# Optimization experiments

Hardware: AMD Instinct MI355X
Metric: run time of the kernel (lower is better)

## Reference

```python
import jax, jax.numpy as jnp
import numpy as np

EMBED_DIM = 1024
NUM_HEADS = 16
HEAD_DIM = EMBED_DIM // NUM_HEADS


def setup_inputs() -> dict:
    key = jax.random.key(0)
    ks = jax.random.split(key, 7)
    B, S, E = 2, 2048, EMBED_DIM
    # xavier_uniform bound for square [E, E] weight
    bound = float(np.sqrt(6.0 / (E + E)))
    mkw = lambda k: jax.random.uniform(k, (E, E), jnp.float32, -bound, bound)
    return {
        "query": jax.random.normal(ks[0], (B, S, E), jnp.float32),
        "key": jax.random.normal(ks[1], (B, S, E), jnp.float32),
        "value": jax.random.normal(ks[2], (B, S, E), jnp.float32),
        "Wq": mkw(ks[3]),
        "Wk": mkw(ks[4]),
        "Wv": mkw(ks[5]),
        "Wo": mkw(ks[6]),
    }


def reference(query, key, value, Wq, Wk, Wv, Wo):
    # Chunked sigmoid attention: since sigmoid has no cross-key normalization
    # and all projections are bias-free linear maps, summing per-KV-chunk
    # partial outputs is mathematically identical to the full computation:
    #   out = (sigmoid(scale * Q K^T) @ V) @ Wo^T
    B, L, E = query.shape
    H, D = NUM_HEADS, HEAD_DIM
    scale = D ** -0.5
    q = (query @ Wq.T).reshape(B, L, H, D) * scale   # [B,L,H,D]
    k = (key @ Wk.T).reshape(B, -1, H, D)            # [B,S,H,D]
    v = (value @ Wv.T).reshape(B, -1, H, D)          # [B,S,H,D]
    scores = jax.nn.sigmoid(jnp.einsum('blhd,bshd->bhls', q, k))  # [B,H,L,S]
    o = jnp.einsum('bhls,bshd->blhd', scores, v).reshape(B, L, E)
    return o @ Wo.T
```

## Files before the change

kernel.cpp:

```cpp
#include <hip/hip_runtime.h>

typedef float f32x4 __attribute__((ext_vector_type(4)));
typedef float f32x16 __attribute__((ext_vector_type(16)));
typedef __bf16 bf16x4 __attribute__((ext_vector_type(4)));
typedef __bf16 bf16x8 __attribute__((ext_vector_type(8)));

constexpr int E = 1024;
constexpr int S = 2048;
constexpr int Bsz = 2;
constexpr int H = 16;
constexpr int Dh = 64;
constexpr int M = Bsz * S;

#define GLOAD_LDS16(g, l)                                                                 \
  __builtin_amdgcn_global_load_lds((const __attribute__((address_space(1))) void*)(g),    \
                                   (__attribute__((address_space(3))) void*)(l), 16, 0, 0)

__device__ __forceinline__ unsigned pk2(float a, float b) {
  union { __bf16 h[2]; unsigned u; } r;
  r.h[0] = (__bf16)a; r.h[1] = (__bf16)b;
  return r.u;
}

__global__ __launch_bounds__(256) void convert_bf16(
    const float* __restrict__ q, const float* __restrict__ k,
    const float* __restrict__ v, const float* __restrict__ wq,
    const float* __restrict__ wk, const float* __restrict__ wv,
    const float* __restrict__ wo, __bf16* __restrict__ aq,
    __bf16* __restrict__ ak, __bf16* __restrict__ av,
    __bf16* __restrict__ wqkv, __bf16* __restrict__ wob) {
  const int id = blockIdx.y;
  const float* src;
  __bf16* dst;
  int n;
  float scale = 1.0f;
  switch (id) {
    case 0: src = q;  dst = aq;             n = M * E; break;
    case 1: src = k;  dst = ak;             n = M * E; break;
    case 2: src = v;  dst = av;             n = M * E; break;
    case 3: src = wq; dst = wqkv;           n = E * E; scale = -0.18033688f; break;
    case 4: src = wk; dst = wqkv + E * E;   n = E * E; break;
    case 5: src = wv; dst = wqkv + 2 * E * E; n = E * E; break;
    default: src = wo; dst = wob;           n = E * E; break;
  }
  const int stride = gridDim.x * 256 * 8;
  for (int i = (blockIdx.x * 256 + threadIdx.x) * 8; i < n; i += stride) {
    f32x4 a = *reinterpret_cast<const f32x4*>(&src[i]);
    f32x4 b = *reinterpret_cast<const f32x4*>(&src[i + 4]);
    bf16x8 o;
    o[0] = (__bf16)(a[0] * scale); o[1] = (__bf16)(a[1] * scale);
    o[2] = (__bf16)(a[2] * scale); o[3] = (__bf16)(a[3] * scale);
    o[4] = (__bf16)(b[0] * scale); o[5] = (__bf16)(b[1] * scale);
    o[6] = (__bf16)(b[2] * scale); o[7] = (__bf16)(b[3] * scale);
    *reinterpret_cast<bf16x8*>(&dst[i]) = o;
  }
}

template <int TM, int MODE>
__global__ __launch_bounds__(256) void gemm_bf16nt(
    const __bf16* __restrict__ A0, const __bf16* __restrict__ A1,
    const __bf16* __restrict__ A2, const __bf16* __restrict__ Bw,
    void* __restrict__ C0, void* __restrict__ C1, void* __restrict__ C2) {
  constexpr int MI = TM / 32;
  __shared__ __bf16 As[TM][64];
  __shared__ __bf16 Bs[128][64];

  const int t    = threadIdx.x;
  const int lane = t & 63;
  const int wid  = t >> 6;
  const int wr   = (wid >> 1) * (TM / 2);
  const int wc   = (wid & 1) * 64;
  const int r16  = lane & 15;
  const int tm   = blockIdx.y * TM;
  const int tn   = blockIdx.x * 128;
  const int which = tn >> 10;

  const __bf16* Ab = (MODE == 0) ? (which == 0 ? A0 : which == 1 ? A1 : A2) : A0;

  f32x4 acc[MI][4] = {};

  for (int kt = 0; kt < E / 64; ++kt) {
    const int k0 = kt * 64;
    __syncthreads();
    constexpr int ACH = TM / 8;
    constexpr int NCH = ACH + 16;
#pragma unroll
    for (int c = wid; c < NCH; c += 4) {
      const bool isA = c < ACH;
      const int cc   = isA ? c : c - ACH;
      const int L    = cc * 1024 + lane * 16;
      const int row  = L >> 7;
      const int sw   = ((L >> 4) & 7) ^ (row & 7);
      const __bf16* src = isA ? &Ab[(size_t)(tm + row) * E + k0 + sw * 8]
                              : &Bw[(size_t)(tn + row) * E + k0 + sw * 8];
      char* dst = (isA ? (char*)As : (char*)Bs) + cc * 1024;
      GLOAD_LDS16(src, dst);
    }
    __syncthreads();
#pragma unroll
    for (int kc = 0; kc < 2; ++kc) {
      bf16x8 af[MI], bfv[4];
#pragma unroll
      for (int mi = 0; mi < MI; ++mi) {
        int row = wr + mi * 16 + r16;
        int g   = (kc * 4 + (lane >> 4)) ^ (row & 7);
        af[mi] = *reinterpret_cast<const bf16x8*>(&As[row][g * 8]);
      }
#pragma unroll
      for (int ni = 0; ni < 4; ++ni) {
        int row = wc + ni * 16 + r16;
        int g   = (kc * 4 + (lane >> 4)) ^ (row & 7);
        bfv[ni] = *reinterpret_cast<const bf16x8*>(&Bs[row][g * 8]);
      }
#pragma unroll
      for (int mi = 0; mi < MI; ++mi)
#pragma unroll
        for (int ni = 0; ni < 4; ++ni)
          acc[mi][ni] = __builtin_amdgcn_mfma_f32_16x16x32_bf16(af[mi], bfv[ni],
                                                                acc[mi][ni], 0, 0, 0);
    }
  }

#pragma unroll
  for (int mi = 0; mi < MI; ++mi) {
#pragma unroll
    for (int ni = 0; ni < 4; ++ni) {
#pragma unroll
      for (int j = 0; j < 4; ++j) {
        float v = acc[mi][ni][j];
        int m = tm + wr + mi * 16 + ((lane >> 4) << 2) + j;
        int n = tn + wc + ni * 16 + r16;
        if constexpr (MODE == 0) {
          int nl = n & 1023;
          int b = m >> 11, s = m & 2047, h = nl >> 6, d = nl & 63;
          __bf16* Cout = which == 0 ? (__bf16*)C0 : which == 1 ? (__bf16*)C1
                                                              : (__bf16*)C2;
          if (which < 2) {
            Cout[((size_t)(b * H + h) * S + s) * Dh + d] = (__bf16)v;
          } else {
            int ssw = (s & ~12) | ((s & 4) << 1) | ((s & 8) >> 1);
            Cout[((size_t)(b * H + h) * Dh + d) * S + ssw] = (__bf16)v;
          }
        } else {
          ((float*)C0)[(size_t)m * E + n] = v;
        }
      }
    }
  }
}

__global__ __launch_bounds__(256) void attn_sigmoid(const __bf16* __restrict__ Q,
                                                    const __bf16* __restrict__ K,
                                                    const __bf16* __restrict__ Vt,
                                                    __bf16* __restrict__ O) {
  __shared__ char smem[32768];

  const int t     = threadIdx.x;
  const int lane  = t & 63;
  const int wid   = t >> 6;
  const int l31   = lane & 31;
  const int hh    = lane >> 5;
  const int qgrp  = wid & 1;
  const int shalf = wid >> 1;
  const int q0    = blockIdx.x * 64;
  const int h     = blockIdx.y;
  const int b     = blockIdx.z;

  const __bf16* Qh = Q + (size_t)(b * H + h) * S * Dh;
  const __bf16* Kh = K + (size_t)(b * H + h) * S * Dh;
  const __bf16* Vh = Vt + (size_t)(b * H + h) * Dh * S;

  char* const myBase = smem + shalf * 16384;

  const __bf16* kSrc = Kh + (size_t)(shalf * 1024 + (lane >> 3)) * Dh +
                       (((lane & 7) ^ (lane >> 3)) * 8);
  const __bf16* vSrc = Vh + (size_t)(lane >> 2) * S + shalf * 1024 +
                       (((lane & 3) ^ ((lane >> 3) & 3)) * 8);

  auto stage = [&](int it, int buf) {
    char* dst = myBase + buf * 8192;
    if (qgrp == 0) {
#pragma unroll
      for (int j = 0; j < 4; ++j)
        GLOAD_LDS16(kSrc + it * 2048 + j * 512, dst + j * 1024);
    } else {
#pragma unroll
      for (int j = 0; j < 4; ++j)
        GLOAD_LDS16(vSrc + it * 32 + (size_t)j * 16 * S, dst + 4096 + j * 1024);
    }
  };

  bf16x8 Qf[4];
#pragma unroll
  for (int kc = 0; kc < 4; ++kc)
    Qf[kc] = *reinterpret_cast<const bf16x8*>(
        &Qh[(size_t)(q0 + qgrp * 32 + l31) * Dh + kc * 16 + hh * 8]);

  stage(0, 0);
  stage(1, 1);

  f32x16 ot0 = {}, ot1 = {};

#pragma unroll 2
  for (int it = 0; it < 32; ++it) {
    const int buf = it & 1;
    if (it + 1 < 32) {
      asm volatile("s_waitcnt vmcnt(4)" ::: "memory");
    } else {
      asm volatile("s_waitcnt vmcnt(0)" ::: "memory");
    }
    __builtin_amdgcn_s_barrier();
    __builtin_amdgcn_sched_barrier(0);

    const __bf16* Kb = (const __bf16*)(myBase + buf * 8192);
    const __bf16* Vb = (const __bf16*)(myBase + buf * 8192 + 4096);

    bf16x8 kf[4], vf[4];
#pragma unroll
    for (int kc = 0; kc < 4; ++kc) {
      int x = (2 * kc + hh) ^ (l31 & 7);
      kf[kc] = *reinterpret_cast<const bf16x8*>(&Kb[l31 * 64 + x * 8]);
    }
#pragma unroll
    for (int kc2 = 0; kc2 < 2; ++kc2)
#pragma unroll
      for (int dblk = 0; dblk < 2; ++dblk) {
        int row = dblk * 32 + l31;
        int x   = (2 * kc2 + hh) ^ ((l31 >> 1) & 3);
        vf[kc2 * 2 + dblk] = *reinterpret_cast<const bf16x8*>(&Vb[row * 32 + x * 8]);
      }

    f32x16 sacc = {};
    __builtin_amdgcn_s_setprio(1);
#pragma unroll
    for (int kc = 0; kc < 4; ++kc)
      sacc = __builtin_amdgcn_mfma_f32_32x32x16_bf16(kf[kc], Qf[kc], sacc, 0, 0, 0);
    __builtin_amdgcn_s_setprio(0);

    bf16x8 F[2];
    {
      union { unsigned u[4]; bf16x8 v; } fu[2];
#pragma unroll
      for (int kc2 = 0; kc2 < 2; ++kc2) {
#pragma unroll
        for (int jj = 0; jj < 4; ++jj) {
          float ya = sacc[kc2 * 8 + 2 * jj];
          float yb = sacc[kc2 * 8 + 2 * jj + 1];
          float pa = __builtin_amdgcn_rcpf(1.0f + __builtin_amdgcn_exp2f(ya));
          float pb = __builtin_amdgcn_rcpf(1.0f + __builtin_amdgcn_exp2f(yb));
          fu[kc2].u[jj] = pk2(pa, pb);
        }
        F[kc2] = fu[kc2].v;
      }
    }

    __builtin_amdgcn_s_setprio(1);
    ot0 = __builtin_amdgcn_mfma_f32_32x32x16_bf16(vf[0], F[0], ot0, 0, 0, 0);
    ot1 = __builtin_amdgcn_mfma_f32_32x32x16_bf16(vf[1], F[0], ot1, 0, 0, 0);
    ot0 = __builtin_amdgcn_mfma_f32_32x32x16_bf16(vf[2], F[1], ot0, 0, 0, 0);
    ot1 = __builtin_amdgcn_mfma_f32_32x32x16_bf16(vf[3], F[1], ot1, 0, 0, 0);
    __builtin_amdgcn_s_setprio(0);

    __builtin_amdgcn_sched_barrier(0);
    __builtin_amdgcn_s_barrier();
    if (it + 2 < 32) stage(it + 2, buf);
  }

  __syncthreads();

  const int q = qgrp * 32 + l31;
  {
    char* Ps = smem;
    if (shalf == 1) {
#pragma unroll
      for (int dblk = 0; dblk < 2; ++dblk)
#pragma unroll
        for (int rp = 0; rp < 4; ++rp) {
          int gg = dblk * 8 + rp * 2 + hh;
          int r  = rp * 4;
          f32x4 v;
          v[0] = dblk ? ot1[r]     : ot0[r];
          v[1] = dblk ? ot1[r + 1] : ot0[r + 1];
          v[2] = dblk ? ot1[r + 2] : ot0[r + 2];
          v[3] = dblk ? ot1[r + 3] : ot0[r + 3];
          *reinterpret_cast<f32x4*>(Ps + q * 256 + ((gg ^ (q & 7)) * 16)) = v;
        }
    }
    __syncthreads();
    if (shalf == 0) {
#pragma unroll
      for (int dblk = 0; dblk < 2; ++dblk)
#pragma unroll
        for (int rp = 0; rp < 4; ++rp) {
          int gg = dblk * 8 + rp * 2 + hh;
          int r  = rp * 4;
          f32x4 v = *reinterpret_cast<const f32x4*>(Ps + q * 256 + ((gg ^ (q & 7)) * 16));
          if (dblk) {
            ot1[r] += v[0]; ot1[r + 1] += v[1]; ot1[r + 2] += v[2]; ot1[r + 3] += v[3];
          } else {
            ot0[r] += v[0]; ot0[r + 1] += v[1]; ot0[r + 2] += v[2]; ot0[r + 3] += v[3];
          }
        }
    }
  }
  __syncthreads();

  __bf16* Os = (__bf16*)smem;
  if (shalf == 0) {
    int row = q;
#pragma unroll
    for (int dblk = 0; dblk < 2; ++dblk)
#pragma unroll
      for (int rp = 0; rp < 4; ++rp) {
        int r  = rp * 4;
        int g  = dblk * 4 + rp;
        int by = row * 128 + ((g ^ (row & 7)) * 16) + hh * 8;
        float a0 = dblk ? ot1[r]     : ot0[r];
        float a1 = dblk ? ot1[r + 1] : ot0[r + 1];
        float a2 = dblk ? ot1[r + 2] : ot0[r + 2];
        float a3 = dblk ? ot1[r + 3] : ot0[r + 3];
        unsigned long long val =
            (unsigned long long)pk2(a0, a1) | ((unsigned long long)pk2(a2, a3) << 32);
        *reinterpret_cast<unsigned long long*>((char*)Os + by) = val;
      }
  }
  __syncthreads();
#pragma unroll
  for (int i = 0; i < 2; ++i) {
    int c   = i * 256 + t;
    int row = c >> 3;
    int ch  = c & 7;
    bf16x8 v = *reinterpret_cast<const bf16x8*>(
        (char*)Os + row * 128 + ((ch ^ (row & 7)) * 16));
    *reinterpret_cast<bf16x8*>(&O[((size_t)(b * S) + q0 + row) * E + h * Dh + ch * 8]) = v;
  }
}

extern "C" void kernel_launch(void* const* d_in, const int* in_sizes, int n_in,
                              void* d_out, int out_size, void* d_ws, size_t ws_size,
                              hipStream_t stream) {
  const float* query = (const float*)d_in[0];
  const float* key_  = (const float*)d_in[1];
  const float* value = (const float*)d_in[2];
  const float* Wq    = (const float*)d_in[3];
  const float* Wk    = (const float*)d_in[4];
  const float* Wv    = (const float*)d_in[5];
  const float* Wo    = (const float*)d_in[6];

  char* ws = (char*)d_ws;
  __bf16* aq   = (__bf16*)(ws);
  __bf16* ak   = (__bf16*)(ws + ((size_t)8 << 20));
  __bf16* av   = (__bf16*)(ws + ((size_t)16 << 20));
  __bf16* wqkv = (__bf16*)(ws + ((size_t)24 << 20));
  __bf16* wob  = (__bf16*)(ws + ((size_t)30 << 20));
  __bf16* pq   = (__bf16*)(ws + ((size_t)32 << 20));
  __bf16* pk   = (__bf16*)(ws + ((size_t)40 << 20));
  __bf16* pvt  = (__bf16*)(ws + ((size_t)48 << 20));
  __bf16* ob   = (__bf16*)(ws);

  convert_bf16<<<dim3(512, 7), 256, 0, stream>>>(query, key_, value, Wq, Wk, Wv,
                                                 Wo, aq, ak, av, wqkv, wob);

  gemm_bf16nt<128, 0><<<dim3(3072 / 128, M / 128), 256, 0, stream>>>(
      aq, ak, av, wqkv, pq, pk, pvt);

  attn_sigmoid<<<dim3(S / 64, H, Bsz), 256, 0, stream>>>(pq, pk, pvt, ob);

  gemm_bf16nt<64, 2><<<dim3(E / 128, M / 64), 256, 0, stream>>>(
      ob, nullptr, nullptr, wob, (float*)d_out, nullptr, nullptr);
}
```

Measured before the change: 152.3 us.

## Fold split-KV partial sums into the output projection GEMM

The attention kernel now splits the KV range across separate 128-thread blocks instead of across waves in one block. Each block writes its bf16 partial output into one half of a 2048-wide buffer. The Wo GEMM runs over K=2048 and reuses the same weight columns for both halves, so the cross-wave LDS reduction and its extra barriers disappear. In exchange the output GEMM does twice the K work, the partial sums are rounded to bf16 before they are added, and the intermediate buffer doubles in size.

```diff
diff --git a/kernel.cpp b/kernel.cpp
--- a/kernel.cpp
+++ b/kernel.cpp
@@ -11,6 +11,7 @@
 constexpr int H = 16;
 constexpr int Dh = 64;
 constexpr int M = Bsz * S;
+constexpr int E2 = 2048;
 
 #define GLOAD_LDS16(g, l)                                                                 \
   __builtin_amdgcn_global_load_lds((const __attribute__((address_space(1))) void*)(g),    \
@@ -56,7 +57,7 @@
   }
 }
 
-template <int TM, int MODE>
+template <int TM, int MODE, int KS>
 __global__ __launch_bounds__(256) void gemm_bf16nt(
     const __bf16* __restrict__ A0, const __bf16* __restrict__ A1,
     const __bf16* __restrict__ A2, const __bf16* __restrict__ Bw,
@@ -79,8 +80,9 @@
 
   f32x4 acc[MI][4] = {};
 
-  for (int kt = 0; kt < E / 64; ++kt) {
-    const int k0 = kt * 64;
+  for (int kt = 0; kt < KS / 64; ++kt) {
+    const int k0  = kt * 64;
+    const int k0b = k0 & 1023;
     __syncthreads();
     constexpr int ACH = TM / 8;
     constexpr int NCH = ACH + 16;
@@ -91,8 +93,8 @@
       const int L    = cc * 1024 + lane * 16;
       const int row  = L >> 7;
       const int sw   = ((L >> 4) & 7) ^ (row & 7);
-      const __bf16* src = isA ? &Ab[(size_t)(tm + row) * E + k0 + sw * 8]
-                              : &Bw[(size_t)(tn + row) * E + k0 + sw * 8];
+      const __bf16* src = isA ? &Ab[(size_t)(tm + row) * KS + k0 + sw * 8]
+                              : &Bw[(size_t)(tn + row) * 1024 + k0b + sw * 8];
       char* dst = (isA ? (char*)As : (char*)Bs) + cc * 1024;
       GLOAD_LDS16(src, dst);
     }
@@ -149,36 +151,34 @@
   }
 }
 
-__global__ __launch_bounds__(256) void attn_sigmoid(const __bf16* __restrict__ Q,
-                                                    const __bf16* __restrict__ K,
-                                                    const __bf16* __restrict__ Vt,
-                                                    __bf16* __restrict__ O) {
-  __shared__ char smem[32768];
-
-  const int t     = threadIdx.x;
-  const int lane  = t & 63;
-  const int wid   = t >> 6;
-  const int l31   = lane & 31;
-  const int hh    = lane >> 5;
-  const int qgrp  = wid & 1;
-  const int shalf = wid >> 1;
-  const int q0    = blockIdx.x * 64;
-  const int h     = blockIdx.y;
-  const int b     = blockIdx.z;
+__global__ __launch_bounds__(128, 4) void attn_sigmoid(const __bf16* __restrict__ Q,
+                                                       const __bf16* __restrict__ K,
+                                                       const __bf16* __restrict__ Vt,
+                                                       __bf16* __restrict__ O) {
+  __shared__ char smem[16384];
+
+  const int t    = threadIdx.x;
+  const int lane = t & 63;
+  const int qgrp = t >> 6;
+  const int l31  = lane & 31;
+  const int hh   = lane >> 5;
+  const int qt   = blockIdx.x >> 1;
+  const int ss   = blockIdx.x & 1;
+  const int q0   = qt * 64;
+  const int h    = blockIdx.y;
+  const int b    = blockIdx.z;
 
   const __bf16* Qh = Q + (size_t)(b * H + h) * S * Dh;
   const __bf16* Kh = K + (size_t)(b * H + h) * S * Dh;
   const __bf16* Vh = Vt + (size_t)(b * H + h) * Dh * S;
 
-  char* const myBase = smem + shalf * 16384;
-
-  const __bf16* kSrc = Kh + (size_t)(shalf * 1024 + (lane >> 3)) * Dh +
+  const __bf16* kSrc = Kh + (size_t)(ss * 1024 + (lane >> 3)) * Dh +
                        (((lane & 7) ^ (lane >> 3)) * 8);
-  const __bf16* vSrc = Vh + (size_t)(lane >> 2) * S + shalf * 1024 +
+  const __bf16* vSrc = Vh + (size_t)(lane >> 2) * S + ss * 1024 +
                        (((lane & 3) ^ ((lane >> 3) & 3)) * 8);
 
   auto stage = [&](int it, int buf) {
-    char* dst = myBase + buf * 8192;
+    char* dst = smem + buf * 8192;
     if (qgrp == 0) {
 #pragma unroll
       for (int j = 0; j < 4; ++j)
@@ -212,8 +212,8 @@
     __builtin_amdgcn_s_barrier();
     __builtin_amdgcn_sched_barrier(0);
 
-    const __bf16* Kb = (const __bf16*)(myBase + buf * 8192);
-    const __bf16* Vb = (const __bf16*)(myBase + buf * 8192 + 4096);
+    const __bf16* Kb = (const __bf16*)(smem + buf * 8192);
+    const __bf16* Vb = (const __bf16*)(smem + buf * 8192 + 4096);
 
     bf16x8 kf[4], vf[4];
 #pragma unroll
@@ -266,48 +266,9 @@
     if (it + 2 < 32) stage(it + 2, buf);
   }
 
-  __syncthreads();
-
-  const int q = qgrp * 32 + l31;
+  __bf16* Os = (__bf16*)smem;
   {
-    char* Ps = smem;
-    if (shalf == 1) {
-#pragma unroll
-      for (int dblk = 0; dblk < 2; ++dblk)
-#pragma unroll
-        for (int rp = 0; rp < 4; ++rp) {
-          int gg = dblk * 8 + rp * 2 + hh;
-          int r  = rp * 4;
-          f32x4 v;
-          v[0] = dblk ? ot1[r]     : ot0[r];
-          v[1] = dblk ? ot1[r + 1] : ot0[r + 1];
-          v[2] = dblk ? ot1[r + 2] : ot0[r + 2];
-          v[3] = dblk ? ot1[r + 3] : ot0[r + 3];
-          *reinterpret_cast<f32x4*>(Ps + q * 256 + ((gg ^ (q & 7)) * 16)) = v;
-        }
-    }
-    __syncthreads();
-    if (shalf == 0) {
-#pragma unroll
-      for (int dblk = 0; dblk < 2; ++dblk)
-#pragma unroll
-        for (int rp = 0; rp < 4; ++rp) {
-          int gg = dblk * 8 + rp * 2 + hh;
-          int r  = rp * 4;
-          f32x4 v = *reinterpret_cast<const f32x4*>(Ps + q * 256 + ((gg ^ (q & 7)) * 16));
-          if (dblk) {
-            ot1[r] += v[0]; ot1[r + 1] += v[1]; ot1[r + 2] += v[2]; ot1[r + 3] += v[3];
-          } else {
-            ot0[r] += v[0]; ot0[r + 1] += v[1]; ot0[r + 2] += v[2]; ot0[r + 3] += v[3];
-          }
-        }
-    }
-  }
-  __syncthreads();
-
-  __bf16* Os = (__bf16*)smem;
-  if (shalf == 0) {
-    int row = q;
+    int row = qgrp * 32 + l31;
 #pragma unroll
     for (int dblk = 0; dblk < 2; ++dblk)
 #pragma unroll
@@ -326,13 +287,14 @@
   }
   __syncthreads();
 #pragma unroll
-  for (int i = 0; i < 2; ++i) {
-    int c   = i * 256 + t;
+  for (int i = 0; i < 4; ++i) {
+    int c   = i * 128 + t;
     int row = c >> 3;
     int ch  = c & 7;
     bf16x8 v = *reinterpret_cast<const bf16x8*>(
         (char*)Os + row * 128 + ((ch ^ (row & 7)) * 16));
-    *reinterpret_cast<bf16x8*>(&O[((size_t)(b * S) + q0 + row) * E + h * Dh + ch * 8]) = v;
+    *reinterpret_cast<bf16x8*>(
+        &O[((size_t)(b * S) + q0 + row) * E2 + ss * 1024 + h * Dh + ch * 8]) = v;
   }
 }
 
@@ -361,11 +323,11 @@
   convert_bf16<<<dim3(512, 7), 256, 0, stream>>>(query, key_, value, Wq, Wk, Wv,
                                                  Wo, aq, ak, av, wqkv, wob);
 
-  gemm_bf16nt<128, 0><<<dim3(3072 / 128, M / 128), 256, 0, stream>>>(
+  gemm_bf16nt<128, 0, 1024><<<dim3(3072 / 128, M / 128), 256, 0, stream>>>(
       aq, ak, av, wqkv, pq, pk, pvt);
 
-  attn_sigmoid<<<dim3(S / 64, H, Bsz), 256, 0, stream>>>(pq, pk, pvt, ob);
-
-  gemm_bf16nt<64, 2><<<dim3(E / 128, M / 64), 256, 0, stream>>>(
+  attn_sigmoid<<<dim3(S / 32, H, Bsz), 128, 0, stream>>>(pq, pk, pvt, ob);
+
+  gemm_bf16nt<64, 2, 2048><<<dim3(E / 128, M / 64), 256, 0, stream>>>(
       ob, nullptr, nullptr, wob, (float*)d_out, nullptr, nullptr);
 }
```

New measurement: 157.5 us. 3.4% more time.
